# Kernel tuning notes

Measured on AMD Instinct MI355X. Metric: run time of the kernel, lower is better.

The kernel has to match this reference:

```python
import jax, jax.numpy as jnp
import numpy as np

VOCAB, EMB, HID, DSEM, TK, B, MAX_OOV = 50000, 128, 512, 256, 400, 64, 100


def _linear(x, W, b=None):
    y = x @ W.T
    return y if b is None else y + b


def setup_inputs() -> dict:
    key = jax.random.key(0)
    ks = jax.random.split(key, 32)
    s = 0.02
    inp = {
        "y_t_1": jax.random.randint(ks[0], (B,), 0, VOCAB),
        "s_h": jax.random.normal(ks[1], (1, B, HID)) * 0.1,
        "s_c": jax.random.normal(ks[2], (1, B, HID)) * 0.1,
        "encoder_outputs": jax.random.normal(ks[3], (B, TK, 2 * HID)) * 0.1,
        "encoder_feature": jax.random.normal(ks[4], (B * TK, 2 * HID)) * 0.1,
        "enc_padding_mask": jnp.ones((B, TK), jnp.float32),
        "c_t_1": jax.random.normal(ks[5], (B, 2 * HID)) * 0.1,
        "extra_zeros": jnp.zeros((B, MAX_OOV), jnp.float32),
        "enc_batch_extend_vocab": jax.random.randint(ks[6], (B, TK), 0, VOCAB + MAX_OOV),
        "coverage": jax.random.uniform(ks[7], (B, TK)),
        "step": 1,
        "ri": jax.random.normal(ks[8], (B, TK, 2 * DSEM)) * 0.1,
        # parameters (torch Linear convention: weight is (out, in))
        "emb_W": jax.random.normal(ks[9], (VOCAB, EMB)) * s,
        "Ws_W": jax.random.normal(ks[10], (2 * HID, 2 * HID)) * s,
        "Ws_b": jax.random.normal(ks[11], (2 * HID,)) * s,
        "v_W": jax.random.normal(ks[12], (1, 2 * HID)) * s,
        "Wc_W": jax.random.normal(ks[13], (2 * HID, 1)) * s,
        "Wr_W": jax.random.normal(ks[14], (2 * HID, 2 * DSEM)) * s,
        "xc_W": jax.random.normal(ks[15], (EMB, 2 * HID + EMB)) * s,
        "xc_b": jax.random.normal(ks[16], (EMB,)) * s,
        "W_ih": jax.random.uniform(ks[17], (4 * HID, EMB), minval=-0.02, maxval=0.02),
        "W_hh": jax.random.uniform(ks[18], (4 * HID, HID), minval=-0.02, maxval=0.02),
        "b_ih": jnp.concatenate([jnp.zeros(HID), jnp.ones(HID), jnp.zeros(2 * HID)]),
        "b_hh": jnp.zeros((4 * HID,), jnp.float32),
        "pg_W": jax.random.normal(ks[19], (1, 4 * HID + EMB)) * s,
        "pg_b": jax.random.normal(ks[20], (1,)) * s,
        "o1_W": jax.random.normal(ks[21], (HID, 3 * HID)) * s,
        "o1_b": jax.random.normal(ks[22], (HID,)) * s,
        "o2_W": jax.random.normal(ks[23], (VOCAB, HID)) * s,
        "o2_b": jax.random.normal(ks[24], (VOCAB,)) * s,
    }
    return inp


def _attention(s_t_hat, encoder_outputs, encoder_feature, enc_padding_mask, coverage, ri,
               Ws_W, Ws_b, v_W, Wc_W, Wr_W):
    b, t_k, n = encoder_outputs.shape
    dec_fea = _linear(s_t_hat, Ws_W, Ws_b)                     # (b, 2h)
    att = encoder_feature.reshape(b, t_k, n) + dec_fea[:, None, :]
    att = att + coverage[..., None] * Wc_W[:, 0]                # coverage feature
    scores = jnp.tanh(att) @ v_W[0]                             # (b, t_k)
    attn = jax.nn.softmax(scores, axis=1) * enc_padding_mask
    attn = attn / attn.sum(1, keepdims=True)
    c_t = jnp.einsum('bt,btn->bn', attn, encoder_outputs)
    coverage_next = coverage + attn
    # structural attention (not renormalized in the original)
    att2 = jnp.einsum('btd,nd->btn', ri, Wr_W) + dec_fea[:, None, :]
    scores2 = jnp.tanh(att2) @ v_W[0]
    a_struct = jax.nn.softmax(scores2, axis=1) * enc_padding_mask
    c_struct = jnp.einsum('bt,btn->bn', a_struct, encoder_outputs)
    return c_t, attn, coverage_next, c_struct, a_struct


def reference(y_t_1, s_h, s_c, encoder_outputs, encoder_feature, enc_padding_mask,
              c_t_1, extra_zeros, enc_batch_extend_vocab, coverage, step, ri,
              emb_W, Ws_W, Ws_b, v_W, Wc_W, Wr_W, xc_W, xc_b,
              W_ih, W_hh, b_ih, b_hh, pg_W, pg_b, o1_W, o1_b, o2_W, o2_b):
    b = y_t_1.shape[0]
    # embed + context projection
    y_emb = emb_W[y_t_1]                                        # (b, emb)
    x = _linear(jnp.concatenate([c_t_1, y_emb], 1), xc_W, xc_b)  # (b, emb)
    # single-step LSTM (torch gate order i,f,g,o)
    h0, c0 = s_h[0], s_c[0]
    gates = x @ W_ih.T + b_ih + h0 @ W_hh.T + b_hh
    i, f, g, o = jnp.split(gates, 4, axis=1)
    c_new = jax.nn.sigmoid(f) * c0 + jax.nn.sigmoid(i) * jnp.tanh(g)
    h_new = jax.nn.sigmoid(o) * jnp.tanh(c_new)
    s_t_hat = jnp.concatenate([h_new, c_new], 1)                # (b, 2h)
    c_t, attn_dist, coverage_next, c_struct, _ = _attention(
        s_t_hat, encoder_outputs, encoder_feature, enc_padding_mask, coverage, ri,
        Ws_W, Ws_b, v_W, Wc_W, Wr_W)
    coverage_out = coverage_next  # training / step>0 path
    # pointer-generator gate
    p_gen = jax.nn.sigmoid(_linear(jnp.concatenate([c_struct, s_t_hat, x], 1), pg_W, pg_b))
    out = _linear(jnp.concatenate([h_new, c_struct], 1), o1_W, o1_b)
    out = _linear(out, o2_W, o2_b)
    vocab_dist = jax.nn.softmax(out, axis=1)
    vocab_dist_ = p_gen * vocab_dist
    attn_ = (1.0 - p_gen) * attn_dist
    ext = jnp.concatenate([vocab_dist_, extra_zeros], 1)        # (b, vocab+oov)
    rows = jnp.arange(b)[:, None]
    final_dist = ext.at[rows, enc_batch_extend_vocab].add(attn_)
    return (final_dist, h_new[None], c_new[None], c_t, attn_dist, p_gen, coverage_out)
```

## Files before the change

kernel.cpp:

```cpp
#include <hip/hip_runtime.h>
#include <hip/hip_bf16.h>
#include <math.h>

#define BATCH  64
#define EMB    128
#define HID    512
#define TK     400
#define VOCAB  50000
#define MAX_OOV 100
#define VEXT   50100
#define H2     1024
#define K_RI   512

typedef short  bf16x8 __attribute__((ext_vector_type(8)));
typedef float  f32x4  __attribute__((ext_vector_type(4)));
typedef unsigned short u16x8 __attribute__((ext_vector_type(8)));

__device__ __forceinline__ unsigned short f2b(float f){
  unsigned u = __float_as_uint(f);
  u += 0x7fffu + ((u >> 16) & 1u);
  return (unsigned short)(u >> 16);
}
__device__ __forceinline__ float sigm(float x){ return 1.0f/(1.0f+expf(-x)); }
__device__ __forceinline__ float clampf(float x, float lo, float hi){ return fminf(fmaxf(x, lo), hi); }
__device__ __forceinline__ float fast_tanh(float x){
  float e = __expf(2.f*x);
  return 1.f - 2.f/(e + 1.f);
}
__device__ __forceinline__ bf16x8 ld_frag(const unsigned short* p){
  return __builtin_bit_cast(bf16x8, *(const u16x8*)p);
}
__device__ __forceinline__ u16x8 cvt8(const float4 a, const float4 b){
  u16x8 r;
  r[0]=f2b(a.x); r[1]=f2b(a.y); r[2]=f2b(a.z); r[3]=f2b(a.w);
  r[4]=f2b(b.x); r[5]=f2b(b.y); r[6]=f2b(b.z); r[7]=f2b(b.w);
  return r;
}

#define WS_X        0
#define WS_H        8192
#define WS_STHAT    73728
#define WS_DECFEA   139264
#define WS_SCORES   204800
#define WS_SCORES2  230400
#define WS_ATTN     256000
#define WS_ASTRUCT  281600
#define WS_CSTRUCT  307200
#define WS_PGEN     372736
#define WS_OUT1BF   372800
#define WS_ROWMAX   389184
#define WS_ROWSUM   389248

#define OUT_FINAL 0
#define OUT_H     3206400
#define OUT_C     3239168
#define OUT_CT    3271936
#define OUT_ATTN  3337472
#define OUT_PGEN  3363072
#define OUT_COV   3363136
#define OUT_WR16  131072
#define CTX_CT    0
#define CTX_CS    262144

__global__ __launch_bounds__(256) void k_wrcvt(const float* __restrict__ Wr,
    unsigned short* __restrict__ WrF){
  int t = blockIdx.x*256 + threadIdx.x;
  int lane = t & 63;
  int f    = (t >> 6) & 15;
  int nb   = t >> 10;
  int r  = nb*16 + (lane & 15);
  int k0 = f*32 + (lane >> 4)*8;
  const float4* p = (const float4*)(Wr + (size_t)r*512 + k0);
  *(u16x8*)(WrF + (size_t)t*8) = cvt8(p[0], p[1]);
}

__global__ __launch_bounds__(256) void k_embx(
    const int* __restrict__ y, const float* __restrict__ embW,
    const float* __restrict__ ct1, const float* __restrict__ xcW,
    const float* __restrict__ xcb, float* __restrict__ ws)
{
  __shared__ float vec[1152];
  int b = blockIdx.x, q = blockIdx.y, tid = threadIdx.x;
  int yb = y[b];
  for (int i = tid; i < 1024; i += 256) vec[i] = ct1[b*1024+i];
  if (tid < 128) vec[1024+tid] = embW[(size_t)yb*128+tid];
  __syncthreads();
  int wave = tid>>6, lane = tid&63;
  #pragma unroll 2
  for (int oo = 0; oo < 8; ++oo){
    int o = q*32 + wave*8 + oo;
    const float* row = xcW + (size_t)o*1152;
    float acc = 0.f;
    #pragma unroll
    for (int i=0;i<18;i++) acc += row[lane + 64*i] * vec[lane + 64*i];
    for (int off=32; off>0; off>>=1) acc += __shfl_down(acc, off);
    if (lane==0) ws[WS_X + b*128 + o] = xcb[o] + acc;
  }
}

__global__ __launch_bounds__(256) void k_gates(
    const float* __restrict__ Wih, const float* __restrict__ Whh,
    const float* __restrict__ bih, const float* __restrict__ bhh,
    const float* __restrict__ sh, const float* __restrict__ ws,
    float* __restrict__ gates)
{
  __shared__ float xh[640];
  int b = blockIdx.x, gc = blockIdx.y, tid = threadIdx.x;
  for (int i=tid;i<128;i+=256) xh[i] = ws[WS_X + b*128 + i];
  for (int i=tid;i<512;i+=256) xh[128+i] = sh[b*512+i];
  __syncthreads();
  int wave = tid>>6, lane = tid&63;
  int gbase = gc*128 + wave*32;
  for (int gg=0; gg<32; ++gg){
    int g = gbase + gg;
    const float* ri = Wih + (size_t)g*128;
    const float* rh = Whh + (size_t)g*512;
    float acc = ri[lane]*xh[lane] + ri[lane+64]*xh[lane+64];
    #pragma unroll
    for (int i=0;i<8;i++) acc += rh[lane + 64*i] * xh[128 + lane + 64*i];
    for (int off=32; off>0; off>>=1) acc += __shfl_down(acc, off);
    if (lane==0) gates[b*2048 + g] = acc + bih[g] + bhh[g];
  }
}

__global__ __launch_bounds__(256) void k_lstmpt(
    const float* __restrict__ gates, const float* __restrict__ sc,
    float* __restrict__ ws, float* __restrict__ outh, float* __restrict__ outc)
{
  int b = blockIdx.x, tid = threadIdx.x;
  const float* g = gates + b*2048;
  for (int j = tid; j < 512; j += 256){
    float ig = sigm(g[j]),       fg = sigm(g[512+j]);
    float gg = tanhf(g[1024+j]), og = sigm(g[1536+j]);
    float c0 = sc[b*512+j];
    float cn = fg*c0 + ig*gg;
    float hn = og*tanhf(cn);
    ws[WS_H + b*512+j] = hn;
    ws[WS_STHAT + b*1024 + j] = hn; ws[WS_STHAT + b*1024 + 512 + j] = cn;
    outh[b*512+j] = hn; outc[b*512+j] = cn;
  }
}

__global__ __launch_bounds__(256) void k_decfea(const float* __restrict__ WsW,
    const float* __restrict__ Wsb, float* __restrict__ ws){
  __shared__ float st[1024];
  int b = blockIdx.x, q = blockIdx.y, tid = threadIdx.x;
  for (int i=tid;i<1024;i+=256) st[i] = ws[WS_STHAT + b*1024 + i];
  __syncthreads();
  int wave = tid>>6, lane = tid&63;
  for (int oo=0; oo<64; ++oo){
    int n = q*256 + wave*64 + oo;
    const float* row = WsW + (size_t)n*1024;
    float acc = 0.f;
    #pragma unroll
    for (int i=0;i<16;i++) acc += row[lane + 64*i] * st[lane + 64*i];
    for (int off=32; off>0; off>>=1) acc += __shfl_down(acc, off);
    if (lane==0) ws[WS_DECFEA + b*1024 + n] = Wsb[n] + acc;
  }
}

__global__ __launch_bounds__(256) void k_scores1(const float* __restrict__ ef,
    const float* __restrict__ cov, const float* __restrict__ vW,
    const float* __restrict__ WcW, float* __restrict__ ws){
  __shared__ float df[1024], vv[1024], wc[1024];
  int b = blockIdx.x, tid = threadIdx.x;
  for (int i=tid;i<1024;i+=256){ df[i]=ws[WS_DECFEA+b*1024+i]; vv[i]=vW[i]; wc[i]=WcW[i]; }
  __syncthreads();
  int wave = tid>>6, lane = tid&63;
  int t = blockIdx.y*4 + wave;
  float cv = cov[b*400+t];
  const float4* e = (const float4*)(ef + (size_t)(b*400+t)*1024 + lane*16);
  float4 e0 = e[0], e1 = e[1], e2 = e[2], e3 = e[3];
  float ebuf[16] = {e0.x,e0.y,e0.z,e0.w, e1.x,e1.y,e1.z,e1.w,
                    e2.x,e2.y,e2.z,e2.w, e3.x,e3.y,e3.z,e3.w};
  float acc = 0.f;
  int base = lane*16;
  #pragma unroll
  for (int j=0;j<16;j++){ int n=base+j; acc += fast_tanh(ebuf[j] + df[n] + cv*wc[n]) * vv[n]; }
  for (int off=32; off>0; off>>=1) acc += __shfl_down(acc, off, 64);
  if (lane==0) ws[WS_SCORES + b*400 + t] = clampf(acc, -64.f, 64.f);
}

__global__ __launch_bounds__(256) void k_scores2(const float* __restrict__ ri,
    const unsigned short* __restrict__ WrF, const float* __restrict__ vW,
    float* __restrict__ ws){
  int tid = threadIdx.x, lane = tid & 63, w = tid >> 6;
  int m0 = blockIdx.x*64 + w*16;
  int fr = lane & 15, fq8 = (lane >> 4)*8;
  int cq = lane >> 4, cr = lane & 15;

  bf16x8 a[16];
  {
    const float* p = ri + (size_t)(m0 + fr)*K_RI + fq8;
    #pragma unroll
    for (int f=0; f<16; f++){
      float4 x0 = *(const float4*)(p + f*32);
      float4 x1 = *(const float4*)(p + f*32 + 4);
      a[f] = __builtin_bit_cast(bf16x8, cvt8(x0, x1));
    }
  }

  const float* decfea = ws + WS_DECFEA;
  int dfo[4];
  #pragma unroll
  for (int rg=0; rg<4; rg++) dfo[rg] = ((m0 + cq*4 + rg)/400)*1024;

  float sa[4] = {0.f,0.f,0.f,0.f};
  const unsigned short* bl = WrF + lane*8;

  for (int it=0; it<32; ++it){
    const unsigned short* b0 = bl + (size_t)(2*it)*8192;
    const unsigned short* b1 = b0 + 8192;
    f32x4 c0a={0.f,0.f,0.f,0.f}, c0b={0.f,0.f,0.f,0.f};
    f32x4 c1a={0.f,0.f,0.f,0.f}, c1b={0.f,0.f,0.f,0.f};
    #pragma unroll
    for (int f=0; f<16; f+=2){
      bf16x8 x0 = ld_frag(b0 + f*512), y0 = ld_frag(b0 + f*512 + 512);
      bf16x8 x1 = ld_frag(b1 + f*512), y1 = ld_frag(b1 + f*512 + 512);
      c0a = __builtin_amdgcn_mfma_f32_16x16x32_bf16(a[f],   x0, c0a, 0,0,0);
      c1a = __builtin_amdgcn_mfma_f32_16x16x32_bf16(a[f],   x1, c1a, 0,0,0);
      c0b = __builtin_amdgcn_mfma_f32_16x16x32_bf16(a[f+1], y0, c0b, 0,0,0);
      c1b = __builtin_amdgcn_mfma_f32_16x16x32_bf16(a[f+1], y1, c1b, 0,0,0);
    }
    int col0 = it*32 + cr, col1 = col0 + 16;
    float v0 = vW[col0], v1 = vW[col1];
    #pragma unroll
    for (int rg=0; rg<4; rg++){
      float t0 = c0a[rg] + c0b[rg] + decfea[dfo[rg] + col0];
      float t1 = c1a[rg] + c1b[rg] + decfea[dfo[rg] + col1];
      sa[rg] += fast_tanh(t0)*v0 + fast_tanh(t1)*v1;
    }
  }
  #pragma unroll
  for (int rg=0; rg<4; rg++){
    float v = sa[rg];
    v += __shfl_xor(v, 1); v += __shfl_xor(v, 2);
    v += __shfl_xor(v, 4); v += __shfl_xor(v, 8);
    sa[rg] = v;
  }
  if (cr == 0){
    #pragma unroll
    for (int rg=0; rg<4; rg++)
      ws[WS_SCORES2 + m0 + cq*4 + rg] = clampf(sa[rg], -64.f, 64.f);
  }
}

__global__ __launch_bounds__(256) void k_softmax(const float* __restrict__ mask,
    const float* __restrict__ covin, float* __restrict__ ws,
    float* __restrict__ out){
  __shared__ float s1[400], s2[400], mk[400], red[256];
  int b = blockIdx.x, tid = threadIdx.x;
  for (int i=tid;i<400;i+=256){
    s1[i]=ws[WS_SCORES+b*400+i]; s2[i]=ws[WS_SCORES2+b*400+i]; mk[i]=mask[b*400+i];
  }
  __syncthreads();
  float lm = -1e30f;
  for (int i=tid;i<400;i+=256) lm = fmaxf(lm, s1[i]);
  red[tid]=lm; __syncthreads();
  for (int off=128;off>0;off>>=1){ if (tid<off) red[tid]=fmaxf(red[tid],red[tid+off]); __syncthreads(); }
  float mx1 = red[0]; __syncthreads();
  float ls=0.f;
  for (int i=tid;i<400;i+=256){ float e=__expf(s1[i]-mx1); s1[i]=e; ls+=e; }
  red[tid]=ls; __syncthreads();
  for (int off=128;off>0;off>>=1){ if (tid<off) red[tid]+=red[tid+off]; __syncthreads(); }
  float sum1 = red[0]; __syncthreads();
  float la=0.f;
  for (int i=tid;i<400;i+=256){ float a=(s1[i]/sum1)*mk[i]; s1[i]=a; la+=a; }
  red[tid]=la; __syncthreads();
  for (int off=128;off>0;off>>=1){ if (tid<off) red[tid]+=red[tid+off]; __syncthreads(); }
  float sumA = red[0]; __syncthreads();
  for (int i=tid;i<400;i+=256){
    float attn = s1[i]/sumA;
    ws[WS_ATTN + b*400 + i] = attn;
    out[OUT_ATTN + b*400 + i] = attn;
    out[OUT_COV  + b*400 + i] = covin[b*400+i] + attn;
  }
  float lm2 = -1e30f;
  for (int i=tid;i<400;i+=256) lm2 = fmaxf(lm2, s2[i]);
  red[tid]=lm2; __syncthreads();
  for (int off=128;off>0;off>>=1){ if (tid<off) red[tid]=fmaxf(red[tid],red[tid+off]); __syncthreads(); }
  float mx2 = red[0]; __syncthreads();
  float ls2=0.f;
  for (int i=tid;i<400;i+=256){ float e=__expf(s2[i]-mx2); s2[i]=e; ls2+=e; }
  red[tid]=ls2; __syncthreads();
  for (int off=128;off>0;off>>=1){ if (tid<off) red[tid]+=red[tid+off]; __syncthreads(); }
  float sum2 = red[0]; __syncthreads();
  for (int i=tid;i<400;i+=256) ws[WS_ASTRUCT + b*400 + i] = (s2[i]/sum2)*mk[i];
}

__global__ __launch_bounds__(256) void k_context(const float* __restrict__ eo,
    const float* __restrict__ ws, float* __restrict__ outp){
  __shared__ float at[100], as2[100];
  int b = blockIdx.x, tid = threadIdx.x;
  int n = blockIdx.y*256 + tid;
  int tz = blockIdx.z;
  for (int i=tid;i<100;i+=256){
    at[i]  = ws[WS_ATTN    + b*400 + tz*100 + i];
    as2[i] = ws[WS_ASTRUCT + b*400 + tz*100 + i];
  }
  __syncthreads();
  const float* p = eo + (size_t)b*400*1024 + (size_t)tz*100*1024 + n;
  float a1=0.f, a2=0.f;
  #pragma unroll 4
  for (int t=0;t<100;t++){
    float e = p[(size_t)t*1024];
    a1 += at[t]*e; a2 += as2[t]*e;
  }
  outp[CTX_CT + tz*65536 + b*1024 + n] = a1;
  outp[CTX_CS + tz*65536 + b*1024 + n] = a2;
}

__global__ __launch_bounds__(256) void k_ctxsum(float* __restrict__ ws,
    float* __restrict__ out){
  int b = blockIdx.x, tid = threadIdx.x;
  int n = tid*4;
  float4 ct = {0.f,0.f,0.f,0.f}, cs = {0.f,0.f,0.f,0.f};
  #pragma unroll
  for (int tz=0;tz<4;tz++){
    float4 a = *(const float4*)(out + CTX_CT + tz*65536 + b*1024 + n);
    float4 c = *(const float4*)(out + CTX_CS + tz*65536 + b*1024 + n);
    ct.x+=a.x; ct.y+=a.y; ct.z+=a.z; ct.w+=a.w;
    cs.x+=c.x; cs.y+=c.y; cs.z+=c.z; cs.w+=c.w;
  }
  *(float4*)(out + OUT_CT + b*1024 + n) = ct;
  *(float4*)(ws + WS_CSTRUCT + b*1024 + n) = cs;
}

__global__ __launch_bounds__(256) void k_pgen(const float* __restrict__ pgW,
    const float* __restrict__ pgb, float* __restrict__ ws,
    float* __restrict__ out){
  __shared__ float red[256];
  int b=blockIdx.x, tid=threadIdx.x;
  float a=0.f;
  for (int i=tid;i<2176;i+=256){
    float x;
    if (i<1024)      x = ws[WS_CSTRUCT + b*1024 + i];
    else if (i<2048) x = ws[WS_STHAT   + b*1024 + (i-1024)];
    else             x = ws[WS_X       + b*128  + (i-2048)];
    a += x * pgW[i];
  }
  red[tid]=a; __syncthreads();
  for (int off=128;off>0;off>>=1){ if(tid<off) red[tid]+=red[tid+off]; __syncthreads(); }
  if (tid==0){
    float p = sigm(red[0] + pgb[0]);
    ws[WS_PGEN+b]=p; out[OUT_PGEN+b]=p;
  }
}

__global__ __launch_bounds__(256) void k_out1(const float* __restrict__ o1W,
    const float* __restrict__ o1b, float* __restrict__ ws){
  __shared__ float in1[1536];
  int b=blockIdx.x, q=blockIdx.y, tid=threadIdx.x;
  for (int i=tid;i<512;i+=256)  in1[i]     = ws[WS_H + b*512 + i];
  for (int i=tid;i<1024;i+=256) in1[512+i] = ws[WS_CSTRUCT + b*1024 + i];
  __syncthreads();
  int wave = tid>>6, lane = tid&63;
  for (int oo=0; oo<64; ++oo){
    int o = q*256 + wave*64 + oo;
    const float* row = o1W + (size_t)o*1536;
    float acc = 0.f;
    #pragma unroll
    for (int i=0;i<24;i++) acc += row[lane + 64*i] * in1[lane + 64*i];
    for (int off=32; off>0; off>>=1) acc += __shfl_down(acc, off);
    if (lane==0) ((unsigned short*)(ws + WS_OUT1BF))[b*512 + o] = f2b(o1b[o] + acc);
  }
}

__global__ __launch_bounds__(256) void k_o2(float* __restrict__ ws,
    const float* __restrict__ o2W, const float* __restrict__ o2b,
    float* __restrict__ out){
  __shared__ __align__(16) unsigned short As[64][72];
  __shared__ __align__(16) unsigned short Bs[64][72];
  int tid=threadIdx.x;
  int n0 = blockIdx.x*64;
  int lane=tid&63, wave=tid>>6, wm=wave&1, wn=wave>>1;
  int lrow=tid>>2, lcol=(tid&3)*16;
  const unsigned short* out1 = (const unsigned short*)(ws + WS_OUT1BF);
  f32x4 acc00={0.f,0.f,0.f,0.f}, acc01={0.f,0.f,0.f,0.f};
  f32x4 acc10={0.f,0.f,0.f,0.f}, acc11={0.f,0.f,0.f,0.f};
  int nrow = n0 + lrow;
  bool bvalid = nrow < VOCAB;
  int fr = lane & 15, fq = (lane >> 4) * 8;
  for (int kc=0;kc<512;kc+=64){
    u16x8 a0 = *(const u16x8*)(out1 + lrow*512 + kc + lcol);
    u16x8 a1 = *(const u16x8*)(out1 + lrow*512 + kc + lcol + 8);
    u16x8 bb0 = {0,0,0,0,0,0,0,0}, bb1 = {0,0,0,0,0,0,0,0};
    if (bvalid){
      const float4* bp = (const float4*)(o2W + (size_t)nrow*512 + kc + lcol);
      float4 b0=bp[0], b1=bp[1], b2=bp[2], b3=bp[3];
      bb0 = cvt8(b0,b1); bb1 = cvt8(b2,b3);
    }
    __syncthreads();
    *(u16x8*)&As[lrow][lcol] = a0;  *(u16x8*)&As[lrow][lcol+8] = a1;
    *(u16x8*)&Bs[lrow][lcol] = bb0; *(u16x8*)&Bs[lrow][lcol+8] = bb1;
    __syncthreads();
    #pragma unroll
    for (int kk=0; kk<64; kk+=32){
      bf16x8 aA = ld_frag(&As[wm*32 +      fr][kk + fq]);
      bf16x8 aB = ld_frag(&As[wm*32 + 16 + fr][kk + fq]);
      bf16x8 bA = ld_frag(&Bs[wn*32 +      fr][kk + fq]);
      bf16x8 bB = ld_frag(&Bs[wn*32 + 16 + fr][kk + fq]);
      acc00 = __builtin_amdgcn_mfma_f32_16x16x32_bf16(aA, bA, acc00, 0,0,0);
      acc01 = __builtin_amdgcn_mfma_f32_16x16x32_bf16(aA, bB, acc01, 0,0,0);
      acc10 = __builtin_amdgcn_mfma_f32_16x16x32_bf16(aB, bA, acc10, 0,0,0);
      acc11 = __builtin_amdgcn_mfma_f32_16x16x32_bf16(aB, bB, acc11, 0,0,0);
    }
  }
  int cq=lane>>4, cr=lane&15;
  #pragma unroll
  for (int i=0;i<2;i++){
    #pragma unroll
    for (int rg=0;rg<4;rg++){
      int row = wm*32 + i*16 + cq*4 + rg;
      int n1 = n0 + wn*32 + cr, n2 = n1+16;
      float v1 = (i==0?acc00[rg]:acc10[rg]);
      float v2 = (i==0?acc01[rg]:acc11[rg]);
      if (n1 < VOCAB) out[(size_t)row*VEXT + n1] = clampf(v1 + o2b[n1], -80.f, 80.f);
      if (n2 < VOCAB) out[(size_t)row*VEXT + n2] = clampf(v2 + o2b[n2], -80.f, 80.f);
    }
  }
}

__global__ __launch_bounds__(256) void k_vsm_stats(float* __restrict__ ws,
    const float* __restrict__ out){
  __shared__ float red[256];
  int b=blockIdx.x, tid=threadIdx.x;
  const float* lg = out + (size_t)b*VEXT;
  float lm=-1e30f;
  for (int i=tid;i<VOCAB;i+=256) lm=fmaxf(lm, lg[i]);
  red[tid]=lm; __syncthreads();
  for (int off=128;off>0;off>>=1){ if(tid<off) red[tid]=fmaxf(red[tid],red[tid+off]); __syncthreads(); }
  float mx=red[0]; __syncthreads();
  float s=0.f;
  for (int i=tid;i<VOCAB;i+=256) s+=__expf(lg[i]-mx);
  red[tid]=s; __syncthreads();
  for (int off=128;off>0;off>>=1){ if(tid<off) red[tid]+=red[tid+off]; __syncthreads(); }
  if (tid==0){ ws[WS_ROWMAX+b]=mx; ws[WS_ROWSUM+b]=red[0]; }
}

__global__ __launch_bounds__(256) void k_vsm_write(const float* __restrict__ ws,
    float* __restrict__ out){
  int b=blockIdx.y;
  int i=blockIdx.x*256+threadIdx.x;
  if (i>=VEXT) return;
  float* p = out + (size_t)b*VEXT + i;
  if (i<VOCAB) *p = ws[WS_PGEN+b]*__expf(*p - ws[WS_ROWMAX+b])/ws[WS_ROWSUM+b];
  else         *p = 0.f;
}

__global__ __launch_bounds__(256) void k_scatter(const int* __restrict__ ebev,
    const float* __restrict__ ws, float* __restrict__ out){
  int idx = blockIdx.x*256+threadIdx.x;
  int b = idx/400;
  float add = (1.f - ws[WS_PGEN+b]) * ws[WS_ATTN+idx];
  int v = ebev[idx];
  atomicAdd(out + (size_t)b*VEXT + v, add);
}

extern "C" void kernel_launch(void* const* d_in, const int* in_sizes, int n_in,
                              void* d_out, int out_size, void* d_ws, size_t ws_size,
                              hipStream_t stream){
  (void)in_sizes; (void)n_in; (void)out_size; (void)ws_size;
  const int*   y_t_1   = (const int*)d_in[0];
  const float* s_h     = (const float*)d_in[1];
  const float* s_c     = (const float*)d_in[2];
  const float* enc_out = (const float*)d_in[3];
  const float* enc_ft  = (const float*)d_in[4];
  const float* mask    = (const float*)d_in[5];
  const float* c_t_1   = (const float*)d_in[6];
  const int*   ebev    = (const int*)d_in[8];
  const float* cover   = (const float*)d_in[9];
  const float* ri      = (const float*)d_in[11];
  const float* embW    = (const float*)d_in[12];
  const float* WsW     = (const float*)d_in[13];
  const float* Wsb     = (const float*)d_in[14];
  const float* vW      = (const float*)d_in[15];
  const float* WcW     = (const float*)d_in[16];
  const float* WrW     = (const float*)d_in[17];
  const float* xcW     = (const float*)d_in[18];
  const float* xcb     = (const float*)d_in[19];
  const float* Wih     = (const float*)d_in[20];
  const float* Whh     = (const float*)d_in[21];
  const float* bih     = (const float*)d_in[22];
  const float* bhh     = (const float*)d_in[23];
  const float* pgW     = (const float*)d_in[24];
  const float* pgb     = (const float*)d_in[25];
  const float* o1W     = (const float*)d_in[26];
  const float* o1b     = (const float*)d_in[27];
  const float* o2W     = (const float*)d_in[28];
  const float* o2b     = (const float*)d_in[29];
  float* ws  = (float*)d_ws;
  float* out = (float*)d_out;
  float* gates = out;
  unsigned short* Wr16 = (unsigned short*)(out + OUT_WR16);

  k_wrcvt   <<<256,           256,0,stream>>>(WrW, Wr16);
  k_embx    <<<dim3(BATCH,4), 256,0,stream>>>(y_t_1, embW, c_t_1, xcW, xcb, ws);
  k_gates   <<<dim3(BATCH,16),256,0,stream>>>(Wih, Whh, bih, bhh, s_h, ws, gates);
  k_lstmpt  <<<BATCH,         256,0,stream>>>(gates, s_c, ws, out+OUT_H, out+OUT_C);
  k_decfea  <<<dim3(BATCH,4), 256,0,stream>>>(WsW, Wsb, ws);
  k_scores1 <<<dim3(BATCH,100),256,0,stream>>>(enc_ft, cover, vW, WcW, ws);
  k_scores2 <<<400,           256,0,stream>>>(ri, Wr16, vW, ws);
  k_softmax <<<BATCH,         256,0,stream>>>(mask, cover, ws, out);
  k_context <<<dim3(BATCH,4,4),256,0,stream>>>(enc_out, ws, out);
  k_ctxsum  <<<BATCH,         256,0,stream>>>(ws, out);
  k_pgen    <<<BATCH,         256,0,stream>>>(pgW, pgb, ws, out);
  k_out1    <<<dim3(BATCH,2), 256,0,stream>>>(o1W, o1b, ws);
  k_o2      <<<782,           256,0,stream>>>(ws, o2W, o2b, out);
  k_vsm_stats<<<BATCH,        256,0,stream>>>(ws, out);
  k_vsm_write<<<dim3(196,BATCH),256,0,stream>>>(ws, out);
  k_scatter <<<100,           256,0,stream>>>(ebev, ws, out);
}
```

Measured before the change: 410.5 us.

## Double-buffer Wr tiles in LDS for scores2 and split vocab softmax stats

k_scores2 now streams the converted Wr weights into a double-buffered LDS tile using global_load_lds, prefetching the next 16K-element slab while MFMAs run on the current one. Previously every wave read B fragments straight from global memory. Separately, the vocab softmax statistics pass is split into 8 partial chunks per row plus a small combine kernel, giving 512 blocks instead of 64 for better occupancy. The costs are 64KB of LDS per block, a barrier every iteration, and one extra kernel launch. The partial max and sum buffers reuse the scores workspace region.

New measurement: 337.8 us (median of 2 runs). 1.22x faster.

```diff
diff --git a/kernel.cpp b/kernel.cpp
--- a/kernel.cpp
+++ b/kernel.cpp
@@ -50,6 +50,8 @@
 #define WS_OUT1BF   372800
 #define WS_ROWMAX   389184
 #define WS_ROWSUM   389248
+#define WS_PMAX     WS_SCORES
+#define WS_PSUM     (WS_SCORES+512)
 
 #define OUT_FINAL 0
 #define OUT_H     3206400
@@ -184,6 +186,7 @@
 __global__ __launch_bounds__(256) void k_scores2(const float* __restrict__ ri,
     const unsigned short* __restrict__ WrF, const float* __restrict__ vW,
     float* __restrict__ ws){
+  __shared__ __align__(16) unsigned short Bs[2][16384];
   int tid = threadIdx.x, lane = tid & 63, w = tid >> 6;
   int m0 = blockIdx.x*64 + w*16;
   int fr = lane & 15, fq8 = (lane >> 4)*8;
@@ -204,12 +207,30 @@
   int dfo[4];
   #pragma unroll
   for (int rg=0; rg<4; rg++) dfo[rg] = ((m0 + cq*4 + rg)/400)*1024;
-
   float sa[4] = {0.f,0.f,0.f,0.f};
-  const unsigned short* bl = WrF + lane*8;
-
-  for (int it=0; it<32; ++it){
-    const unsigned short* b0 = bl + (size_t)(2*it)*8192;
+
+  #pragma unroll
+  for (int i=0;i<8;i++){
+    int e = (i*256 + tid)*8;
+    __builtin_amdgcn_global_load_lds(
+      (const __attribute__((address_space(1))) unsigned int*)(WrF + e),
+      (__attribute__((address_space(3))) unsigned int*)&Bs[0][e], 16, 0, 0);
+  }
+
+  for (int p=0; p<32; ++p){
+    __syncthreads();
+    if (p < 31){
+      const unsigned short* src = WrF + (size_t)(p+1)*16384;
+      unsigned short* dst = Bs[(p+1)&1];
+      #pragma unroll
+      for (int i=0;i<8;i++){
+        int e = (i*256 + tid)*8;
+        __builtin_amdgcn_global_load_lds(
+          (const __attribute__((address_space(1))) unsigned int*)(src + e),
+          (__attribute__((address_space(3))) unsigned int*)(dst + e), 16, 0, 0);
+      }
+    }
+    const unsigned short* b0 = &Bs[p&1][lane*8];
     const unsigned short* b1 = b0 + 8192;
     f32x4 c0a={0.f,0.f,0.f,0.f}, c0b={0.f,0.f,0.f,0.f};
     f32x4 c1a={0.f,0.f,0.f,0.f}, c1b={0.f,0.f,0.f,0.f};
@@ -222,7 +243,7 @@
       c0b = __builtin_amdgcn_mfma_f32_16x16x32_bf16(a[f+1], y0, c0b, 0,0,0);
       c1b = __builtin_amdgcn_mfma_f32_16x16x32_bf16(a[f+1], y1, c1b, 0,0,0);
     }
-    int col0 = it*32 + cr, col1 = col0 + 16;
+    int col0 = p*32 + cr, col1 = col0 + 16;
     float v0 = vW[col0], v1 = vW[col1];
     #pragma unroll
     for (int rg=0; rg<4; rg++){
@@ -421,21 +442,32 @@
   }
 }
 
-__global__ __launch_bounds__(256) void k_vsm_stats(float* __restrict__ ws,
-    const float* __restrict__ out){
+__global__ __launch_bounds__(256) void k_vsm_part(const float* __restrict__ out,
+    float* __restrict__ ws){
   __shared__ float red[256];
-  int b=blockIdx.x, tid=threadIdx.x;
-  const float* lg = out + (size_t)b*VEXT;
+  int b=blockIdx.x, s=blockIdx.y, tid=threadIdx.x;
+  const float* lg = out + (size_t)b*VEXT + s*6250;
   float lm=-1e30f;
-  for (int i=tid;i<VOCAB;i+=256) lm=fmaxf(lm, lg[i]);
+  for (int i=tid;i<6250;i+=256) lm=fmaxf(lm, lg[i]);
   red[tid]=lm; __syncthreads();
   for (int off=128;off>0;off>>=1){ if(tid<off) red[tid]=fmaxf(red[tid],red[tid+off]); __syncthreads(); }
   float mx=red[0]; __syncthreads();
-  float s=0.f;
-  for (int i=tid;i<VOCAB;i+=256) s+=__expf(lg[i]-mx);
-  red[tid]=s; __syncthreads();
+  float sm=0.f;
+  for (int i=tid;i<6250;i+=256) sm+=__expf(lg[i]-mx);
+  red[tid]=sm; __syncthreads();
   for (int off=128;off>0;off>>=1){ if(tid<off) red[tid]+=red[tid+off]; __syncthreads(); }
-  if (tid==0){ ws[WS_ROWMAX+b]=mx; ws[WS_ROWSUM+b]=red[0]; }
+  if (tid==0){ ws[WS_PMAX + b*8 + s]=mx; ws[WS_PSUM + b*8 + s]=red[0]; }
+}
+
+__global__ __launch_bounds__(64) void k_vsm_comb(float* __restrict__ ws){
+  int b = blockIdx.x;
+  if (threadIdx.x==0){
+    float M=-1e30f;
+    for (int s=0;s<8;s++) M=fmaxf(M, ws[WS_PMAX + b*8 + s]);
+    float S=0.f;
+    for (int s=0;s<8;s++) S += __expf(ws[WS_PMAX + b*8 + s]-M)*ws[WS_PSUM + b*8 + s];
+    ws[WS_ROWMAX+b]=M; ws[WS_ROWSUM+b]=S;
+  }
 }
 
 __global__ __launch_bounds__(256) void k_vsm_write(const float* __restrict__ ws,
@@ -507,7 +539,8 @@
   k_pgen    <<<BATCH,         256,0,stream>>>(pgW, pgb, ws, out);
   k_out1    <<<dim3(BATCH,2), 256,0,stream>>>(o1W, o1b, ws);
   k_o2      <<<782,           256,0,stream>>>(ws, o2W, o2b, out);
-  k_vsm_stats<<<BATCH,        256,0,stream>>>(ws, out);
+  k_vsm_part<<<dim3(BATCH,8), 256,0,stream>>>(out, ws);
+  k_vsm_comb<<<BATCH,         64, 0,stream>>>(ws);
   k_vsm_write<<<dim3(196,BATCH),256,0,stream>>>(ws, out);
   k_scatter <<<100,           256,0,stream>>>(ebev, ws, out);
 }
```
